# Optimization experiments

Hardware: AMD Instinct MI355X
Metric: run time of the kernel (lower is better)

## Reference

```python
import jax, jax.numpy as jnp
import numpy as np

IN_F = 4096
OUT_F = 11008
P8 = 128
P6 = 256
P4 = IN_F - P8 - P6  # 3712


def setup_inputs() -> dict:
    key = jax.random.key(0)
    k1, k2, k3, k4 = jax.random.split(key, 4)
    x = jax.random.normal(k1, (32, 8, IN_F), dtype=jnp.float32)
    W = jax.random.normal(k2, (OUT_F, IN_F), dtype=jnp.float32) * 0.02
    bias = jax.random.normal(k3, (OUT_F,), dtype=jnp.float32) * 0.01
    # channel permutation: first P4 channels -> 4-bit, next P6 -> 6-bit, last P8 -> 8-bit outliers
    reorder_index = jax.random.permutation(k4, IN_F).astype(jnp.int32)
    return {"x": x, "W": W, "bias": bias, "reorder_index": reorder_index}


def _quant(v, bits):
    # symmetric per-row quantization (per-token for acts, per-out-channel for weights)
    qmax = float(2 ** (bits - 1) - 1)
    s = jnp.max(jnp.abs(v), axis=-1, keepdims=True) / qmax
    s = jnp.where(s == 0, jnp.ones_like(s), s)
    q = jnp.round(jnp.clip(v / s, -qmax, qmax))
    return q, s


def reference(x, W, bias, reorder_index):
    bsz, q_len, F = x.shape
    xr = x.reshape(bsz * q_len, F)[:, reorder_index]  # reorder_quantize_x gather
    Wr = W[:, reorder_index]                          # reorder_quantize_w4 gather
    y = jnp.zeros((bsz * q_len, W.shape[0]), dtype=x.dtype)
    start = 0
    for bits, n in ((4, P4), (6, P6), (8, P8)):
        qa, sa = _quant(xr[:, start:start + n], bits)      # [T,n], [T,1]
        qb, sb = _quant(Wr[:, start:start + n], bits)      # [O,n], [O,1]
        # dequantized partial matmul: (qa @ qb.T) * sa * sb.T
        y = y + jnp.einsum('tn,on->to', qa, qb) * (sa * sb.T)
        start += n
    y = y + bias
    return y.reshape(bsz, q_len, -1)
```

## Files before the change

### kernel.cpp

```cpp
#include <hip/hip_runtime.h>
#include <stdint.h>

#define T_ROWS 256
#define KF 4096
#define OF 11008

typedef int   v4i __attribute__((ext_vector_type(4)));
typedef float v4f __attribute__((ext_vector_type(4)));

typedef const __attribute__((address_space(1))) uint8_t* gptr_t;
typedef __attribute__((address_space(3))) uint8_t* lptr_t;

__global__ __launch_bounds__(256) void quant_k(const float* __restrict__ x,
                                               const float* __restrict__ W,
                                               const int* __restrict__ idx,
                                               int8_t* __restrict__ qX,
                                               int8_t* __restrict__ qW,
                                               float* __restrict__ sX,
                                               float* __restrict__ sW) {
    __shared__ float rowbuf[KF];
    __shared__ float lmax[256];
    __shared__ float sm[3];
    const int b = blockIdx.x;
    const int t = threadIdx.x;
    const int w = t >> 6, ln = t & 63;
    const float* src; int8_t* qout; float* scales; int r; int nrows;
    if (b < T_ROWS) { src = x; qout = qX; scales = sX; r = b; nrows = T_ROWS; }
    else           { src = W; qout = qW; scales = sW; r = b - T_ROWS; nrows = OF; }
    const float* row = src + (size_t)r * KF;

#pragma unroll
    for (int j = 0; j < 4; ++j) {
        const uint8_t* srcp = (const uint8_t*)(row + j * 1024 + t * 4);
        __builtin_amdgcn_global_load_lds((gptr_t)srcp, (lptr_t)&rowbuf[j * 1024 + w * 256], 16, 0, 0);
    }

    const int seg = t < 232 ? 0 : (t < 248 ? 1 : 2);
    const float qmax = seg == 0 ? 7.f : (seg == 1 ? 31.f : 127.f);
    int c[16];
#pragma unroll
    for (int i = 0; i < 4; ++i) {
        v4i ci = *(const v4i*)&idx[t * 16 + i * 4];
        c[i*4+0] = ci[0]; c[i*4+1] = ci[1]; c[i*4+2] = ci[2]; c[i*4+3] = ci[3];
    }
    __syncthreads();

    float v[16];
    float mx = 0.f;
#pragma unroll
    for (int i = 0; i < 16; ++i) { v[i] = rowbuf[c[i]]; mx = fmaxf(mx, fabsf(v[i])); }
    lmax[t] = mx;
    __syncthreads();
    if (w == 0) {
        float m = fmaxf(fmaxf(lmax[ln], lmax[ln + 64]), lmax[ln + 128]);
        if (ln < 40) m = fmaxf(m, lmax[ln + 192]);
#pragma unroll
        for (int off = 32; off; off >>= 1) m = fmaxf(m, __shfl_xor(m, off));
        if (ln == 0) sm[0] = m;
    } else if (w == 1) {
        float m = ln < 16 ? lmax[232 + ln] : 0.f;
#pragma unroll
        for (int off = 8; off; off >>= 1) m = fmaxf(m, __shfl_xor(m, off));
        if (ln == 0) sm[1] = m;
    } else if (w == 2) {
        float m = ln < 8 ? lmax[248 + ln] : 0.f;
#pragma unroll
        for (int off = 4; off; off >>= 1) m = fmaxf(m, __shfl_xor(m, off));
        if (ln == 0) sm[2] = m;
    }
    __syncthreads();
    float s = sm[seg] / qmax;
    if (s == 0.f) s = 1.f;
    if (t == 0 || t == 232 || t == 248) scales[seg * nrows + r] = s;
    const float rs = 1.0f / s;
    union { int8_t bb[16]; v4i q; } u;
#pragma unroll
    for (int i = 0; i < 16; ++i) {
        float qv = rintf(fminf(fmaxf(v[i] * rs, -qmax), qmax));
        u.bb[i] = (int8_t)qv;
    }
    *(v4i*)(qout + (size_t)r * KF + t * 16) = u.q;
}

__global__ __launch_bounds__(256, 2)
void gemm_k(const int8_t* __restrict__ qX, const int8_t* __restrict__ qW,
            const float* __restrict__ sX, const float* __restrict__ sW,
            const float* __restrict__ bias, float* __restrict__ out) {
    __shared__ __align__(16) int8_t lB[4][64 * 128];

    const int bid = blockIdx.x;
    const int swz = (bid & 7) * 43 + (bid >> 3);
    const int row0 = (swz & 1) * 128;
    const int col0 = (swz >> 1) * 64;
    const int tid = threadIdx.x;
    const int lane = tid & 63;
    const int w = tid >> 6;
    const int lr = lane >> 3, lc = lane & 7;
    const int kg = lane >> 4;
    const int cr = lane & 15;

    v4i iacc[2][4];
    v4f facc[2][4];
#pragma unroll
    for (int m = 0; m < 2; ++m)
#pragma unroll
        for (int n = 0; n < 4; ++n) {
            iacc[m][n][0]=0; iacc[m][n][1]=0; iacc[m][n][2]=0; iacc[m][n][3]=0;
            facc[m][n][0]=0.f; facc[m][n][1]=0.f; facc[m][n][2]=0.f; facc[m][n][3]=0.f;
        }

    const int8_t* aRow[2];
    aRow[0] = qX + (size_t)(row0 + w * 32 + cr) * KF;
    aRow[1] = qX + (size_t)(row0 + w * 32 + 16 + cr) * KF;

    auto stageB = [&](int slot, int step) {
        const int k0 = step * 128;
        const int sc = (lc ^ lr) << 4;
#pragma unroll
        for (int j = 0; j < 2; ++j) {
            const int brow = j * 32 + w * 8;
            const uint8_t* src = (const uint8_t*)qW + (size_t)(col0 + brow + lr) * KF + k0 + sc;
            __builtin_amdgcn_global_load_lds((gptr_t)src, (lptr_t)&lB[slot][brow * 128], 16, 0, 0);
        }
    };

    auto loadA = [&](v4i (&a)[2][2], int step) {
        const int kb = step * 128 + kg * 16;
#pragma unroll
        for (int m = 0; m < 2; ++m)
#pragma unroll
            for (int kk = 0; kk < 2; ++kk) {
                const int8_t* p = aRow[m] + kb + kk * 64;
                asm volatile("global_load_dwordx4 %0, %1, off"
                             : "=v"(a[m][kk]) : "v"(p) : "memory");
            }
    };

    auto flush = [&](int seg) {
#pragma unroll
        for (int m = 0; m < 2; ++m) {
            float sa[4];
#pragma unroll
            for (int rr = 0; rr < 4; ++rr)
                sa[rr] = sX[seg * T_ROWS + row0 + w * 32 + m * 16 + ((lane >> 4) << 2) + rr];
#pragma unroll
            for (int n = 0; n < 4; ++n) {
                const float sb = sW[seg * OF + col0 + n * 16 + (lane & 15)];
#pragma unroll
                for (int rr = 0; rr < 4; ++rr) {
                    facc[m][n][rr] += (float)iacc[m][n][rr] * (sa[rr] * sb);
                    iacc[m][n][rr] = 0;
                }
            }
        }
    };

    auto body = [&](int t, v4i (&aCur)[2][2], v4i (&aNext)[2][2]) {
        __builtin_amdgcn_s_barrier();
        if (t + 1 < 32) loadA(aNext, t + 1);
        v4i bf[4][2];
        const int8_t* pb = &lB[t & 3][0];
#pragma unroll
        for (int n = 0; n < 4; ++n) {
            const int brow = n * 16 + cr;
#pragma unroll
            for (int kk = 0; kk < 2; ++kk) {
                const int ch = (kk * 4 + kg) ^ (brow & 7);
                bf[n][kk] = *(const v4i*)(pb + brow * 128 + ch * 16);
            }
        }
        if (t + 3 < 32) stageB((t + 3) & 3, t + 3);
        if (t <= 28)      asm volatile("s_waitcnt vmcnt(8) lgkmcnt(0)" ::: "memory");
        else if (t == 29) asm volatile("s_waitcnt vmcnt(6) lgkmcnt(0)" ::: "memory");
        else if (t == 30) asm volatile("s_waitcnt vmcnt(4) lgkmcnt(0)" ::: "memory");
        else              asm volatile("s_waitcnt vmcnt(0) lgkmcnt(0)" ::: "memory");
        __builtin_amdgcn_sched_barrier(0);
#pragma unroll
        for (int kk = 0; kk < 2; ++kk)
#pragma unroll
            for (int m = 0; m < 2; ++m)
#pragma unroll
                for (int n = 0; n < 4; ++n)
                    iacc[m][n] = __builtin_amdgcn_mfma_i32_16x16x64_i8(aCur[m][kk], bf[n][kk], iacc[m][n], 0, 0, 0);
        if (t == 28) flush(0);
        else if (t == 30) flush(1);
    };

    v4i aA[2][2], aB[2][2];
    stageB(0, 0);
    stageB(1, 1);
    loadA(aA, 0);
    stageB(2, 2);
    asm volatile("s_waitcnt vmcnt(8)" ::: "memory");

    for (int tt = 0; tt < 32; tt += 2) {
        body(tt,     aA, aB);
        body(tt + 1, aB, aA);
    }
    flush(2);

#pragma unroll
    for (int m = 0; m < 2; ++m)
#pragma unroll
        for (int n = 0; n < 4; ++n) {
            const int colg = col0 + n * 16 + (lane & 15);
            const float bv = bias[colg];
#pragma unroll
            for (int rr = 0; rr < 4; ++rr) {
                const int rowg = row0 + w * 32 + m * 16 + ((lane >> 4) << 2) + rr;
                out[(size_t)rowg * OF + colg] = facc[m][n][rr] + bv;
            }
        }
}

extern "C" void kernel_launch(void* const* d_in, const int* in_sizes, int n_in,
                              void* d_out, int out_size, void* d_ws, size_t ws_size,
                              hipStream_t stream) {
    const float* x    = (const float*)d_in[0];
    const float* W    = (const float*)d_in[1];
    const float* bias = (const float*)d_in[2];
    const int*   ridx = (const int*)d_in[3];
    float* out = (float*)d_out;

    uint8_t* ws = (uint8_t*)d_ws;
    int8_t* qX = (int8_t*)ws;
    int8_t* qW = (int8_t*)(ws + 1048576);
    float*  sX = (float*)(ws + 46137344);
    float*  sW = (float*)(ws + 46140416);

    quant_k<<<T_ROWS + OF, 256, 0, stream>>>(x, W, ridx, qX, qW, sX, sW);
    gemm_k<<<344, 256, 0, stream>>>(qX, qW, sX, sW, bias, out);
}
```

Before: 73.79 us.

## Shrink GEMM block tile to 64x64 and double grid for occupancy

Changes the GEMM block tile from 128x64 to 64x64 (each wave now handles 16 rows instead of 32), doubles the grid to 688 blocks, and raises the launch-bounds occupancy hint to 3 blocks per CU. The wait counts and swizzle are adjusted to match the halved A loads. The aim is more parallelism across the 256 CUs and better latency hiding. In exchange, each B tile is reused over half as many rows, which doubles B (weight) traffic from L2/HBM.

```diff
diff --git a/kernel.cpp b/kernel.cpp
--- a/kernel.cpp
+++ b/kernel.cpp
@@ -82,16 +82,16 @@
     *(v4i*)(qout + (size_t)r * KF + t * 16) = u.q;
 }
 
-__global__ __launch_bounds__(256, 2)
+__global__ __launch_bounds__(256, 3)
 void gemm_k(const int8_t* __restrict__ qX, const int8_t* __restrict__ qW,
             const float* __restrict__ sX, const float* __restrict__ sW,
             const float* __restrict__ bias, float* __restrict__ out) {
     __shared__ __align__(16) int8_t lB[4][64 * 128];
 
     const int bid = blockIdx.x;
-    const int swz = (bid & 7) * 43 + (bid >> 3);
-    const int row0 = (swz & 1) * 128;
-    const int col0 = (swz >> 1) * 64;
+    const int swz = (bid & 7) * 86 + (bid >> 3);
+    const int row0 = (swz & 3) * 64;
+    const int col0 = (swz >> 2) * 64;
     const int tid = threadIdx.x;
     const int lane = tid & 63;
     const int w = tid >> 6;
@@ -99,19 +99,15 @@
     const int kg = lane >> 4;
     const int cr = lane & 15;
 
-    v4i iacc[2][4];
-    v4f facc[2][4];
-#pragma unroll
-    for (int m = 0; m < 2; ++m)
-#pragma unroll
-        for (int n = 0; n < 4; ++n) {
-            iacc[m][n][0]=0; iacc[m][n][1]=0; iacc[m][n][2]=0; iacc[m][n][3]=0;
-            facc[m][n][0]=0.f; facc[m][n][1]=0.f; facc[m][n][2]=0.f; facc[m][n][3]=0.f;
-        }
-
-    const int8_t* aRow[2];
-    aRow[0] = qX + (size_t)(row0 + w * 32 + cr) * KF;
-    aRow[1] = qX + (size_t)(row0 + w * 32 + 16 + cr) * KF;
+    v4i iacc[4];
+    v4f facc[4];
+#pragma unroll
+    for (int n = 0; n < 4; ++n) {
+        iacc[n][0]=0; iacc[n][1]=0; iacc[n][2]=0; iacc[n][3]=0;
+        facc[n][0]=0.f; facc[n][1]=0.f; facc[n][2]=0.f; facc[n][3]=0.f;
+    }
+
+    const int8_t* aRow = qX + (size_t)(row0 + w * 16 + cr) * KF;
 
     auto stageB = [&](int slot, int step) {
         const int k0 = step * 128;
@@ -124,38 +120,33 @@
         }
     };
 
-    auto loadA = [&](v4i (&a)[2][2], int step) {
+    auto loadA = [&](v4i (&a)[2], int step) {
         const int kb = step * 128 + kg * 16;
 #pragma unroll
-        for (int m = 0; m < 2; ++m)
-#pragma unroll
-            for (int kk = 0; kk < 2; ++kk) {
-                const int8_t* p = aRow[m] + kb + kk * 64;
-                asm volatile("global_load_dwordx4 %0, %1, off"
-                             : "=v"(a[m][kk]) : "v"(p) : "memory");
+        for (int kk = 0; kk < 2; ++kk) {
+            const int8_t* p = aRow + kb + kk * 64;
+            asm volatile("global_load_dwordx4 %0, %1, off"
+                         : "=v"(a[kk]) : "v"(p) : "memory");
+        }
+    };
+
+    auto flush = [&](int seg) {
+        float sa[4];
+#pragma unroll
+        for (int rr = 0; rr < 4; ++rr)
+            sa[rr] = sX[seg * T_ROWS + row0 + w * 16 + ((lane >> 4) << 2) + rr];
+#pragma unroll
+        for (int n = 0; n < 4; ++n) {
+            const float sb = sW[seg * OF + col0 + n * 16 + (lane & 15)];
+#pragma unroll
+            for (int rr = 0; rr < 4; ++rr) {
+                facc[n][rr] += (float)iacc[n][rr] * (sa[rr] * sb);
+                iacc[n][rr] = 0;
             }
-    };
-
-    auto flush = [&](int seg) {
-#pragma unroll
-        for (int m = 0; m < 2; ++m) {
-            float sa[4];
-#pragma unroll
-            for (int rr = 0; rr < 4; ++rr)
-                sa[rr] = sX[seg * T_ROWS + row0 + w * 32 + m * 16 + ((lane >> 4) << 2) + rr];
-#pragma unroll
-            for (int n = 0; n < 4; ++n) {
-                const float sb = sW[seg * OF + col0 + n * 16 + (lane & 15)];
-#pragma unroll
-                for (int rr = 0; rr < 4; ++rr) {
-                    facc[m][n][rr] += (float)iacc[m][n][rr] * (sa[rr] * sb);
-                    iacc[m][n][rr] = 0;
-                }
-            }
-        }
-    };
-
-    auto body = [&](int t, v4i (&aCur)[2][2], v4i (&aNext)[2][2]) {
+        }
+    };
+
+    auto body = [&](int t, v4i (&aCur)[2], v4i (&aNext)[2]) {
         __builtin_amdgcn_s_barrier();
         if (t + 1 < 32) loadA(aNext, t + 1);
         v4i bf[4][2];
@@ -170,28 +161,26 @@
             }
         }
         if (t + 3 < 32) stageB((t + 3) & 3, t + 3);
-        if (t <= 28)      asm volatile("s_waitcnt vmcnt(8) lgkmcnt(0)" ::: "memory");
-        else if (t == 29) asm volatile("s_waitcnt vmcnt(6) lgkmcnt(0)" ::: "memory");
-        else if (t == 30) asm volatile("s_waitcnt vmcnt(4) lgkmcnt(0)" ::: "memory");
+        if (t <= 28)      asm volatile("s_waitcnt vmcnt(6) lgkmcnt(0)" ::: "memory");
+        else if (t == 29) asm volatile("s_waitcnt vmcnt(4) lgkmcnt(0)" ::: "memory");
+        else if (t == 30) asm volatile("s_waitcnt vmcnt(2) lgkmcnt(0)" ::: "memory");
         else              asm volatile("s_waitcnt vmcnt(0) lgkmcnt(0)" ::: "memory");
         __builtin_amdgcn_sched_barrier(0);
 #pragma unroll
         for (int kk = 0; kk < 2; ++kk)
 #pragma unroll
-            for (int m = 0; m < 2; ++m)
-#pragma unroll
-                for (int n = 0; n < 4; ++n)
-                    iacc[m][n] = __builtin_amdgcn_mfma_i32_16x16x64_i8(aCur[m][kk], bf[n][kk], iacc[m][n], 0, 0, 0);
+            for (int n = 0; n < 4; ++n)
+                iacc[n] = __builtin_amdgcn_mfma_i32_16x16x64_i8(aCur[kk], bf[n][kk], iacc[n], 0, 0, 0);
         if (t == 28) flush(0);
         else if (t == 30) flush(1);
     };
 
-    v4i aA[2][2], aB[2][2];
+    v4i aA[2], aB[2];
     stageB(0, 0);
     stageB(1, 1);
     loadA(aA, 0);
     stageB(2, 2);
-    asm volatile("s_waitcnt vmcnt(8)" ::: "memory");
+    asm volatile("s_waitcnt vmcnt(6)" ::: "memory");
 
     for (int tt = 0; tt < 32; tt += 2) {
         body(tt,     aA, aB);
@@ -200,17 +189,15 @@
     flush(2);
 
 #pragma unroll
-    for (int m = 0; m < 2; ++m)
-#pragma unroll
-        for (int n = 0; n < 4; ++n) {
-            const int colg = col0 + n * 16 + (lane & 15);
-            const float bv = bias[colg];
-#pragma unroll
-            for (int rr = 0; rr < 4; ++rr) {
-                const int rowg = row0 + w * 32 + m * 16 + ((lane >> 4) << 2) + rr;
-                out[(size_t)rowg * OF + colg] = facc[m][n][rr] + bv;
-            }
-        }
+    for (int n = 0; n < 4; ++n) {
+        const int colg = col0 + n * 16 + (lane & 15);
+        const float bv = bias[colg];
+#pragma unroll
+        for (int rr = 0; rr < 4; ++rr) {
+            const int rowg = row0 + w * 16 + ((lane >> 4) << 2) + rr;
+            out[(size_t)rowg * OF + colg] = facc[n][rr] + bv;
+        }
+    }
 }
 
 extern "C" void kernel_launch(void* const* d_in, const int* in_sizes, int n_in,
@@ -229,5 +216,5 @@
     float*  sW = (float*)(ws + 46140416);
 
     quant_k<<<T_ROWS + OF, 256, 0, stream>>>(x, W, ridx, qX, qW, sX, sW);
-    gemm_k<<<344, 256, 0, stream>>>(qX, qW, sX, sW, bias, out);
+    gemm_k<<<688, 256, 0, stream>>>(qX, qW, sX, sW, bias, out);
 }
```

Result: faster. 68.42 us (median of 2 runs) (-7.3%).
